# Kernel optimization log

Measured on AMD Instinct MI355X. Metric: run time of the kernel, lower is better.

Reference implementation:

```python
import jax, jax.numpy as jnp
import numpy as np

B, C, L, H = 8, 1024, 1024, 16
GROUPS = 32
EPS = 1e-5


def setup_inputs() -> dict:
    key = jax.random.key(0)
    ks = jax.random.split(key, 5)
    return {
        "x": jax.random.normal(ks[0], (B, C, L), dtype=jnp.float32),
        "norm_w": jnp.ones((C,), dtype=jnp.float32),
        "norm_b": jnp.zeros((C,), dtype=jnp.float32),
        "qkv_w": jax.random.normal(ks[1], (3 * C, C), dtype=jnp.float32) * (1.0 / np.sqrt(C)),
        "qkv_b": jax.random.normal(ks[2], (3 * C,), dtype=jnp.float32) * 0.02,
        "proj_w": jax.random.normal(ks[3], (C, C), dtype=jnp.float32) * (1.0 / np.sqrt(C)),
        "proj_b": jax.random.normal(ks[4], (C,), dtype=jnp.float32) * 0.02,
    }


def _group_norm(x, w, b):
    # x: [B, C, L]; GroupNorm over (channels-in-group, length)
    bs, c, l = x.shape
    xg = x.reshape(bs, GROUPS, c // GROUPS, l)
    mean = jnp.mean(xg, axis=(2, 3), keepdims=True)
    var = jnp.var(xg, axis=(2, 3), keepdims=True)
    xn = ((xg - mean) * jax.lax.rsqrt(var + EPS)).reshape(bs, c, l)
    return xn * w[None, :, None] + b[None, :, None]


def reference(x, norm_w, norm_b, qkv_w, qkv_b, proj_w, proj_b):
    b, c, l = x.shape
    ch = c // H  # per-head channels
    x_norm = _group_norm(x, norm_w, norm_b)
    # 1x1 conv == channel matmul: [B, 3C, L]
    qkv = jnp.einsum('oc,bcl->bol', qkv_w, x_norm) + qkv_b[None, :, None]
    # torch layout: reshape(bs*H, 3*ch, L) then split -> per-head [q; k; v]
    qkv = qkv.reshape(b * H, 3 * ch, l)
    q, k, v = qkv[:, :ch], qkv[:, ch:2 * ch], qkv[:, 2 * ch:]
    scale = 1.0 / np.sqrt(np.sqrt(ch))
    # explicit [b*H, L, L] score matrix, softmax in fp32 (matches .float())
    weight = jnp.einsum('bct,bcs->bts', q * scale, k * scale)
    weight = jax.nn.softmax(weight.astype(jnp.float32), axis=-1)
    a = jnp.einsum('bts,bcs->bct', weight, v.astype(jnp.float32))
    h = a.reshape(b, c, l).astype(x.dtype)
    h = jnp.einsum('oc,bcl->bol', proj_w, h) + proj_b[None, :, None]
    return x_norm + h  # tortoise_norm=False branch
```

## Files before the change

### kernel.cpp

```cpp
#include <hip/hip_runtime.h>
#include <cstdint>
#include <cstddef>

#define B_   8
#define C_   1024
#define L_   1024
#define H_   16
#define CH_  64
#define NG_  32
#define CPG_ 32

typedef __bf16 bf16;
typedef _Float16 f16;
typedef bf16  bf16x8 __attribute__((ext_vector_type(8)));
typedef bf16  bf16x4 __attribute__((ext_vector_type(4)));
typedef f16   f16x4  __attribute__((ext_vector_type(4)));
typedef f16   f16x2  __attribute__((ext_vector_type(2)));
typedef float f32x4  __attribute__((ext_vector_type(4)));

#define QSCALE 0.1803368801111203f

__device__ __forceinline__ void async_cp16(void* lds, const void* g) {
  __builtin_amdgcn_global_load_lds((__attribute__((address_space(1))) void*)g,
                                   (__attribute__((address_space(3))) void*)lds,
                                   16, 0, 0);
}

__device__ __forceinline__ f16x2 pk_f16(float a, float b) {
  return __builtin_bit_cast(f16x2, __builtin_amdgcn_cvt_pkrtz(a, b));
}

__device__ __forceinline__ int sw64(int r, int c) {
  return r * 64 + ((c ^ (r & 7)) << 3);
}

__global__ __launch_bounds__(256) void cvt_bf16_kernel(const float* __restrict__ src,
                                                       bf16* __restrict__ dst, int n4) {
  int i = blockIdx.x * 256 + threadIdx.x;
  if (i < n4) {
    float4 f = reinterpret_cast<const float4*>(src)[i];
    bf16x4 o;
    o[0] = (bf16)f.x; o[1] = (bf16)f.y; o[2] = (bf16)f.z; o[3] = (bf16)f.w;
    reinterpret_cast<bf16x4*>(dst)[i] = o;
  }
}

__global__ __launch_bounds__(256) void gn_stats_kernel(const float* __restrict__ x,
                                                       float* __restrict__ stats) {
  const int bg = blockIdx.x >> 3, sl = blockIdx.x & 7;
  const int tid = threadIdx.x;
  const float* xs = x + (size_t)bg * CPG_ * L_;
  const int c = tid >> 3;
  const int lbase = sl * 128 + (tid & 7) * 4;

  float s = 0.f, s2 = 0.f;
  #pragma unroll
  for (int t = 0; t < 4; t++) {
    float4 f = *reinterpret_cast<const float4*>(xs + (size_t)c * L_ + lbase + t * 32);
    s  += f.x + f.y + f.z + f.w;
    s2 += f.x * f.x + f.y * f.y + f.z * f.z + f.w * f.w;
  }
  __shared__ float rs[256], rs2[256];
  rs[tid] = s; rs2[tid] = s2;
  __syncthreads();
  for (int d = 128; d > 0; d >>= 1) {
    if (tid < d) { rs[tid] += rs[tid + d]; rs2[tid] += rs2[tid + d]; }
    __syncthreads();
  }
  if (tid == 0) {
    atomicAdd(&stats[bg * 2],     rs[0]);
    atomicAdd(&stats[bg * 2 + 1], rs2[0]);
  }
}

__global__ __launch_bounds__(256) void gn_apply_kernel(const float* __restrict__ x,
                                                       const float* __restrict__ gw,
                                                       const float* __restrict__ gb,
                                                       const float* __restrict__ stats,
                                                       bf16* __restrict__ xnb,
                                                       bf16* __restrict__ xT) {
  const int bg = blockIdx.x >> 2, l0 = (blockIdx.x & 3) * 256;
  const int b = bg >> 5, g = bg & 31;
  const int tid = threadIdx.x;
  const float* xs = x + (size_t)bg * CPG_ * L_;

  const float mean = stats[bg * 2] * (1.f / 32768.f);
  const float var  = stats[bg * 2 + 1] * (1.f / 32768.f) - mean * mean;
  const float inv  = rsqrtf(var + 1e-5f);

  __shared__ float tile[CPG_][257];
  #pragma unroll 4
  for (int c = 0; c < CPG_; c++) {
    const int gc = g * CPG_ + c;
    const float y = (xs[(size_t)c * L_ + l0 + tid] - mean) * inv * gw[gc] + gb[gc];
    xnb[(size_t)(b * C_ + gc) * L_ + l0 + tid] = (bf16)y;
    tile[c][tid] = y;
  }
  __syncthreads();
  const int c2 = tid & 31, lw = tid >> 5;
  #pragma unroll 4
  for (int jj = 0; jj < 32; jj++) {
    const int l = l0 + jj * 8 + lw;
    xT[(size_t)(b * L_ + l) * C_ + g * CPG_ + c2] = (bf16)tile[c2][jj * 8 + lw];
  }
}

__device__ __forceinline__ void gemm128_bt(const bf16* __restrict__ A,
                                           const bf16* __restrict__ Bt,
                                           int lda, int ldb, int K,
                                           int m0, int n0,
                                           bf16* As, bf16* Bs,
                                           f32x4 acc[4][4]) {
  const int tid  = threadIdx.x;
  const int wave = tid >> 6, lane = tid & 63;
  const int wm = (wave >> 1) * 64, wn = (wave & 1) * 64;
  const int l4 = lane & 15, quad = lane >> 4;
  const int rsub = lane >> 3;
  const int csrc = (((lane & 7) ^ rsub) << 3);

  const bf16* ga = A  + (size_t)(m0 + rsub) * lda + csrc;
  const bf16* gb = Bt + (size_t)(n0 + rsub) * ldb + csrc;

  for (int k0 = 0; k0 < K; k0 += 64) {
    __syncthreads();
    #pragma unroll
    for (int i = wave; i < 16; i += 4) {
      async_cp16(As + i * 512, ga + (size_t)(i * 8) * lda + k0);
      async_cp16(Bs + i * 512, gb + (size_t)(i * 8) * ldb + k0);
    }
    __syncthreads();

    #pragma unroll
    for (int kk = 0; kk < 2; kk++) {
      bf16x8 af[4], bfv[4];
      #pragma unroll
      for (int i = 0; i < 4; i++) {
        af[i] = *reinterpret_cast<const bf16x8*>(As + sw64(wm + i * 16 + l4, kk * 4 + quad));
      }
      #pragma unroll
      for (int j = 0; j < 4; j++) {
        bfv[j] = *reinterpret_cast<const bf16x8*>(Bs + sw64(wn + j * 16 + l4, kk * 4 + quad));
      }
      #pragma unroll
      for (int i = 0; i < 4; i++) {
        #pragma unroll
        for (int j = 0; j < 4; j++) {
          acc[i][j] = __builtin_amdgcn_mfma_f32_16x16x32_bf16(af[i], bfv[j], acc[i][j], 0, 0, 0);
        }
      }
    }
  }
}

__global__ __launch_bounds__(256) void qkv_gemm_kernel(const bf16* __restrict__ Wq,
                                                       const bf16* __restrict__ xT,
                                                       const float* __restrict__ bias,
                                                       bf16* __restrict__ qT,
                                                       bf16* __restrict__ kT,
                                                       f16* __restrict__ vB) {
  __shared__ bf16 As[128 * 64], Bs[128 * 64];
  const int bi = blockIdx.z;
  const int m0 = blockIdx.y * 128, n0 = blockIdx.x * 128;

  f32x4 acc[4][4];
  #pragma unroll
  for (int i = 0; i < 4; i++) {
    #pragma unroll
    for (int j = 0; j < 4; j++) { acc[i][j] = (f32x4){0.f, 0.f, 0.f, 0.f}; }
  }

  gemm128_bt(Wq, xT + (size_t)bi * L_ * C_, C_, C_, C_, m0, n0, As, Bs, acc);

  const int tid = threadIdx.x;
  const int wave = tid >> 6, lane = tid & 63;
  const int wm = (wave >> 1) * 64, wn = (wave & 1) * 64;
  const int l4 = lane & 15, quad = lane >> 4;

  #pragma unroll
  for (int i = 0; i < 4; i++) {
    const int ob = m0 + wm + i * 16 + quad * 4;
    const int h = ob / 192, r = ob % 192;
    const int sec = r >> 6, c = r & 63;
    float bb[4];
    #pragma unroll
    for (int rg = 0; rg < 4; rg++) { bb[rg] = bias[ob + rg]; }
    #pragma unroll
    for (int j = 0; j < 4; j++) {
      const int l = n0 + wn + j * 16 + l4;
      f32x4 a = acc[i][j];
      if (sec == 2) {
        const int e = l & 63, g64 = l >> 6;
        #pragma unroll
        for (int rg = 0; rg < 4; rg++) {
          const int cc = c + rg;
          const int ep = ((((e >> 2) ^ cc) & 15) << 2) | (e & 3);
          vB[(size_t)((bi * H_ + h) * CH_ + cc) * L_ + (g64 << 6) + ep] =
              (f16)(a[rg] + bb[rg]);
        }
      } else {
        const float sc = (sec == 0) ? QSCALE : 1.0f;
        bf16* dst = (sec == 0 ? qT : kT) + (size_t)((bi * H_ + h) * L_ + l) * CH_ + c;
        bf16x4 o;
        #pragma unroll
        for (int rg = 0; rg < 4; rg++) { o[rg] = (bf16)((a[rg] + bb[rg]) * sc); }
        *reinterpret_cast<bf16x4*>(dst) = o;
      }
    }
  }
}

__global__ __launch_bounds__(256, 4) void attn_kernel(const bf16* __restrict__ qT,
                                                      const bf16* __restrict__ kT,
                                                      const f16* __restrict__ vB,
                                                      bf16* __restrict__ aT) {
  const int tid = threadIdx.x, wave = tid >> 6, lane = tid & 63;
  const int l4 = lane & 15, quad = lane >> 4;
  const int rsub = lane >> 3;
  const int csrc = ((lane & 7) ^ rsub) << 3;

  __shared__ char smem[32768];

  const int tile = blockIdx.x;
  const int t0 = (tile & 7) * 128;
  const int hb = tile >> 3;
  const bf16* q = qT + (size_t)hb * L_ * CH_;
  const bf16* k = kT + (size_t)hb * L_ * CH_;
  const f16*  v = vB + (size_t)hb * CH_ * L_;

  {
    const bf16* gq = q + (size_t)t0 * CH_;
    #pragma unroll
    for (int i = wave; i < 16; i += 4) {
      async_cp16(smem + 16384 + i * 1024, gq + (i * 8 + rsub) * 64 + csrc);
    }
    #pragma unroll
    for (int i = wave; i < 8; i += 4) {
      async_cp16(smem + i * 1024, k + (size_t)(i * 8 + rsub) * 64 + csrc);
      async_cp16(smem + 8192 + i * 1024, v + (size_t)(i * 8 + rsub) * L_ + ((lane & 7) << 3));
    }
  }
  __syncthreads();

  bf16x8 bq0[2], bq1[2];
  {
    const bf16* qs = (const bf16*)(smem + 16384);
    #pragma unroll
    for (int u = 0; u < 2; u++) {
      bq0[u] = *reinterpret_cast<const bf16x8*>(qs + sw64(wave * 32 + u * 16 + l4, quad));
      bq1[u] = *reinterpret_cast<const bf16x8*>(qs + sw64(wave * 32 + u * 16 + l4, quad + 4));
    }
  }
  __syncthreads();

  f32x4 oacc[2][4];
  f32x4 lacc[2];
  float m_s[2];
  #pragma unroll
  for (int u = 0; u < 2; u++) {
    #pragma unroll
    for (int ct = 0; ct < 4; ct++) { oacc[u][ct] = (f32x4){0.f, 0.f, 0.f, 0.f}; }
    lacc[u] = (f32x4){0.f, 0.f, 0.f, 0.f};
    m_s[u] = -1e30f;
  }

  const f16x4 vone = {(f16)1.f, (f16)1.f, (f16)1.f, (f16)1.f};

  for (int it = 0; it < 16; it++) {
    const int cur = it & 1;
    if (it < 15) {
      const int s1 = (it + 1) * 64;
      char* nb = smem + (cur ^ 1) * 16384;
      const bf16* gk = k + (size_t)s1 * CH_;
      const f16*  gv = v + s1;
      #pragma unroll
      for (int i = wave; i < 8; i += 4) {
        async_cp16(nb + i * 1024, gk + (size_t)(i * 8 + rsub) * 64 + csrc);
        async_cp16(nb + 8192 + i * 1024, gv + (size_t)(i * 8 + rsub) * L_ + ((lane & 7) << 3));
      }
    }
    const bf16* ksc = (const bf16*)(smem + cur * 16384);
    const f16*  vsc = (const f16*)(smem + cur * 16384 + 8192);

    f32x4 st[2][4];
    #pragma unroll
    for (int j = 0; j < 4; j++) {
      const bf16x8 ak0 = *reinterpret_cast<const bf16x8*>(ksc + sw64(j * 16 + l4, quad));
      const bf16x8 ak1 = *reinterpret_cast<const bf16x8*>(ksc + sw64(j * 16 + l4, quad + 4));
      #pragma unroll
      for (int u = 0; u < 2; u++) {
        f32x4 z = (f32x4){0.f, 0.f, 0.f, 0.f};
        z = __builtin_amdgcn_mfma_f32_16x16x32_bf16(ak0, bq0[u], z, 0, 0, 0);
        z = __builtin_amdgcn_mfma_f32_16x16x32_bf16(ak1, bq1[u], z, 0, 0, 0);
        st[u][j] = z;
      }
    }

    float alpha[2], mn[2];
    #pragma unroll
    for (int u = 0; u < 2; u++) {
      float mx = fmaxf(fmaxf(st[u][0][0], st[u][0][1]), fmaxf(st[u][0][2], st[u][0][3]));
      #pragma unroll
      for (int j = 1; j < 4; j++) {
        mx = fmaxf(mx, fmaxf(fmaxf(st[u][j][0], st[u][j][1]), fmaxf(st[u][j][2], st[u][j][3])));
      }
      mx = fmaxf(mx, __shfl_xor(mx, 16));
      mx = fmaxf(mx, __shfl_xor(mx, 32));
      mn[u] = fmaxf(m_s[u], mx);
      alpha[u] = __builtin_amdgcn_exp2f(m_s[u] - mn[u]);
      m_s[u] = mn[u];
    }

    if (__any(alpha[0] != 1.0f || alpha[1] != 1.0f)) {
      #pragma unroll
      for (int u = 0; u < 2; u++) {
        float ar[4];
        #pragma unroll
        for (int r = 0; r < 4; r++) { ar[r] = __shfl(alpha[u], quad * 4 + r); }
        #pragma unroll
        for (int ct = 0; ct < 4; ct++) {
          #pragma unroll
          for (int r = 0; r < 4; r++) { oacc[u][ct][r] *= ar[r]; }
        }
        #pragma unroll
        for (int r = 0; r < 4; r++) { lacc[u][r] *= ar[r]; }
      }
    }

    f16x4 pa[2][4];
    #pragma unroll
    for (int u = 0; u < 2; u++) {
      #pragma unroll
      for (int j = 0; j < 4; j++) {
        const float p0 = __builtin_amdgcn_exp2f(st[u][j][0] - mn[u]);
        const float p1 = __builtin_amdgcn_exp2f(st[u][j][1] - mn[u]);
        const float p2 = __builtin_amdgcn_exp2f(st[u][j][2] - mn[u]);
        const float p3 = __builtin_amdgcn_exp2f(st[u][j][3] - mn[u]);
        pa[u][j] = __builtin_shufflevector(pk_f16(p0, p1), pk_f16(p2, p3), 0, 1, 2, 3);
        lacc[u] = __builtin_amdgcn_mfma_f32_16x16x16f16(pa[u][j], vone, lacc[u], 0, 0, 0);
      }
    }

    #pragma unroll
    for (int ct = 0; ct < 4; ct++) {
      const int c = ct * 16 + l4;
      #pragma unroll
      for (int j = 0; j < 4; j++) {
        const f16x4 vb = *reinterpret_cast<const f16x4*>(
            vsc + c * 64 + (((4 * j + quad) ^ l4) << 2));
        #pragma unroll
        for (int u = 0; u < 2; u++) {
          oacc[u][ct] = __builtin_amdgcn_mfma_f32_16x16x16f16(pa[u][j], vb, oacc[u][ct], 0, 0, 0);
        }
      }
    }
    __syncthreads();
  }

  const int bi = hb >> 4, h = hb & 15;
  #pragma unroll
  for (int u = 0; u < 2; u++) {
    float linv[4];
    #pragma unroll
    for (int r = 0; r < 4; r++) { linv[r] = 1.f / lacc[u][r]; }
    #pragma unroll
    for (int ct = 0; ct < 4; ct++) {
      #pragma unroll
      for (int r = 0; r < 4; r++) {
        const int t = t0 + wave * 32 + u * 16 + quad * 4 + r;
        const int c = h * CH_ + ct * 16 + l4;
        aT[(size_t)(bi * L_ + t) * C_ + c] = (bf16)(oacc[u][ct][r] * linv[r]);
      }
    }
  }
}

__global__ __launch_bounds__(256) void proj_gemm_kernel(const bf16* __restrict__ Wp,
                                                        const bf16* __restrict__ aT,
                                                        const float* __restrict__ bias,
                                                        const bf16* __restrict__ xnb,
                                                        float* __restrict__ out) {
  __shared__ bf16 As[128 * 64], Bs[128 * 64];
  const int bi = blockIdx.z;
  const int m0 = blockIdx.y * 128, n0 = blockIdx.x * 128;

  f32x4 acc[4][4];
  #pragma unroll
  for (int i = 0; i < 4; i++) {
    #pragma unroll
    for (int j = 0; j < 4; j++) { acc[i][j] = (f32x4){0.f, 0.f, 0.f, 0.f}; }
  }

  gemm128_bt(Wp, aT + (size_t)bi * L_ * C_, C_, C_, C_, m0, n0, As, Bs, acc);

  const int tid = threadIdx.x;
  const int wave = tid >> 6, lane = tid & 63;
  const int wm = (wave >> 1) * 64, wn = (wave & 1) * 64;
  const int l4 = lane & 15, quad = lane >> 4;

  #pragma unroll
  for (int i = 0; i < 4; i++) {
    const int ob = m0 + wm + i * 16 + quad * 4;
    float bb[4];
    #pragma unroll
    for (int rg = 0; rg < 4; rg++) { bb[rg] = bias[ob + rg]; }
    #pragma unroll
    for (int j = 0; j < 4; j++) {
      const int l = n0 + wn + j * 16 + l4;
      #pragma unroll
      for (int rg = 0; rg < 4; rg++) {
        const size_t idx = (size_t)(bi * C_ + ob + rg) * L_ + l;
        out[idx] = acc[i][j][rg] + bb[rg] + (float)xnb[idx];
      }
    }
  }
}

extern "C" void kernel_launch(void* const* d_in, const int* in_sizes, int n_in,
                              void* d_out, int out_size, void* d_ws, size_t ws_size,
                              hipStream_t stream) {
  (void)in_sizes; (void)n_in; (void)out_size; (void)ws_size;
  const float* x      = (const float*)d_in[0];
  const float* norm_w = (const float*)d_in[1];
  const float* norm_b = (const float*)d_in[2];
  const float* qkv_w  = (const float*)d_in[3];
  const float* qkv_b  = (const float*)d_in[4];
  const float* proj_w = (const float*)d_in[5];
  const float* proj_b = (const float*)d_in[6];
  float* out = (float*)d_out;

  char* w = (char*)d_ws;
  auto alloc = [&](size_t bytes) {
    char* p = w;
    w += (bytes + 255) & ~(size_t)255;
    return p;
  };
  bf16*  xnb   = (bf16*)alloc((size_t)B_ * C_ * L_ * 2);
  bf16*  xT    = (bf16*)alloc((size_t)B_ * L_ * C_ * 2);
  bf16*  wq    = (bf16*)alloc((size_t)3 * C_ * C_ * 2);
  bf16*  wp    = (bf16*)alloc((size_t)C_ * C_ * 2);
  bf16*  qT    = (bf16*)alloc((size_t)B_ * H_ * L_ * CH_ * 2);
  bf16*  kT    = (bf16*)alloc((size_t)B_ * H_ * L_ * CH_ * 2);
  f16*   vB    = (f16*)alloc((size_t)B_ * H_ * CH_ * L_ * 2);
  bf16*  aTb   = (bf16*)alloc((size_t)B_ * L_ * C_ * 2);
  float* stats = (float*)alloc((size_t)B_ * NG_ * 2 * 4);

  (void)hipMemsetAsync(stats, 0, (size_t)B_ * NG_ * 2 * 4, stream);
  cvt_bf16_kernel<<<(3 * C_ * C_ / 4) / 256, 256, 0, stream>>>(qkv_w, wq, 3 * C_ * C_ / 4);
  cvt_bf16_kernel<<<(C_ * C_ / 4) / 256, 256, 0, stream>>>(proj_w, wp, C_ * C_ / 4);
  gn_stats_kernel<<<B_ * NG_ * 8, 256, 0, stream>>>(x, stats);
  gn_apply_kernel<<<B_ * NG_ * 4, 256, 0, stream>>>(x, norm_w, norm_b, stats, xnb, xT);
  qkv_gemm_kernel<<<dim3(L_ / 128, 3 * C_ / 128, B_), 256, 0, stream>>>(wq, xT, qkv_b, qT, kT, vB);
  attn_kernel<<<1024, 256, 0, stream>>>(qT, kT, vB, aTb);
  proj_gemm_kernel<<<dim3(L_ / 128, C_ / 128, B_), 256, 0, stream>>>(wp, aTb, proj_b, xnb, out);
}
```

Before: 266.8 us.

## Double-buffer GEMM LDS tiles with K=32 stages and prefetch next tile

The shared bf16 GEMM mainloop changes from single-buffered 64-wide K tiles to double-buffered 32-wide K tiles. The async global-to-LDS copy of the next tile is issued before the MFMAs on the current tile, and a new swizzle suits the 32-column layout. The kernels also declare a minimum of 4 blocks per CU in their launch bounds. The goal is to hide global load latency behind compute and drop one barrier per iteration, at the cost of twice as many loop iterations and tighter register limits.

Measured after the change: 279.1 us. 4.6% more time.

```diff
diff --git a/kernel.cpp b/kernel.cpp
--- a/kernel.cpp
+++ b/kernel.cpp
@@ -30,6 +30,9 @@
   return __builtin_bit_cast(f16x2, __builtin_amdgcn_cvt_pkrtz(a, b));
 }
 
+__device__ __forceinline__ int sw32(int r, int c) {
+  return r * 32 + ((c ^ ((r >> 1) & 3)) << 3);
+}
 __device__ __forceinline__ int sw64(int r, int c) {
   return r * 64 + ((c ^ (r & 7)) << 3);
 }
@@ -115,50 +118,58 @@
   const int wave = tid >> 6, lane = tid & 63;
   const int wm = (wave >> 1) * 64, wn = (wave & 1) * 64;
   const int l4 = lane & 15, quad = lane >> 4;
-  const int rsub = lane >> 3;
-  const int csrc = (((lane & 7) ^ rsub) << 3);
-
-  const bf16* ga = A  + (size_t)(m0 + rsub) * lda + csrc;
-  const bf16* gb = Bt + (size_t)(n0 + rsub) * ldb + csrc;
-
-  for (int k0 = 0; k0 < K; k0 += 64) {
+  const int srow = lane >> 2;
+  const int scol = (((lane & 3) ^ ((srow >> 1) & 3)) << 3);
+
+  const bf16* ga = A  + (size_t)(m0 + wave * 16 + srow) * lda + scol;
+  const bf16* gb = Bt + (size_t)(n0 + wave * 16 + srow) * ldb + scol;
+  const int woff = wave * 512;
+
+  async_cp16(As + woff,        ga);
+  async_cp16(As + 2048 + woff, ga + (size_t)64 * lda);
+  async_cp16(Bs + woff,        gb);
+  async_cp16(Bs + 2048 + woff, gb + (size_t)64 * ldb);
+  __syncthreads();
+
+  for (int k0 = 0; k0 < K; k0 += 32) {
+    const int cur = (k0 >> 5) & 1;
+    if (k0 + 32 < K) {
+      const int nxt = (cur ^ 1) * 4096;
+      async_cp16(As + nxt + woff,        ga + k0 + 32);
+      async_cp16(As + nxt + 2048 + woff, ga + (size_t)64 * lda + k0 + 32);
+      async_cp16(Bs + nxt + woff,        gb + k0 + 32);
+      async_cp16(Bs + nxt + 2048 + woff, gb + (size_t)64 * ldb + k0 + 32);
+    }
+    const bf16* Ac = As + cur * 4096;
+    const bf16* Bc = Bs + cur * 4096;
+
+    bf16x8 af[4], bfv[4];
+    #pragma unroll
+    for (int i = 0; i < 4; i++) {
+      af[i] = *reinterpret_cast<const bf16x8*>(Ac + sw32(wm + i * 16 + l4, quad));
+    }
+    #pragma unroll
+    for (int j = 0; j < 4; j++) {
+      bfv[j] = *reinterpret_cast<const bf16x8*>(Bc + sw32(wn + j * 16 + l4, quad));
+    }
+    #pragma unroll
+    for (int i = 0; i < 4; i++) {
+      #pragma unroll
+      for (int j = 0; j < 4; j++) {
+        acc[i][j] = __builtin_amdgcn_mfma_f32_16x16x32_bf16(af[i], bfv[j], acc[i][j], 0, 0, 0);
+      }
+    }
     __syncthreads();
-    #pragma unroll
-    for (int i = wave; i < 16; i += 4) {
-      async_cp16(As + i * 512, ga + (size_t)(i * 8) * lda + k0);
-      async_cp16(Bs + i * 512, gb + (size_t)(i * 8) * ldb + k0);
-    }
-    __syncthreads();
-
-    #pragma unroll
-    for (int kk = 0; kk < 2; kk++) {
-      bf16x8 af[4], bfv[4];
-      #pragma unroll
-      for (int i = 0; i < 4; i++) {
-        af[i] = *reinterpret_cast<const bf16x8*>(As + sw64(wm + i * 16 + l4, kk * 4 + quad));
-      }
-      #pragma unroll
-      for (int j = 0; j < 4; j++) {
-        bfv[j] = *reinterpret_cast<const bf16x8*>(Bs + sw64(wn + j * 16 + l4, kk * 4 + quad));
-      }
-      #pragma unroll
-      for (int i = 0; i < 4; i++) {
-        #pragma unroll
-        for (int j = 0; j < 4; j++) {
-          acc[i][j] = __builtin_amdgcn_mfma_f32_16x16x32_bf16(af[i], bfv[j], acc[i][j], 0, 0, 0);
-        }
-      }
-    }
-  }
-}
-
-__global__ __launch_bounds__(256) void qkv_gemm_kernel(const bf16* __restrict__ Wq,
-                                                       const bf16* __restrict__ xT,
-                                                       const float* __restrict__ bias,
-                                                       bf16* __restrict__ qT,
-                                                       bf16* __restrict__ kT,
-                                                       f16* __restrict__ vB) {
-  __shared__ bf16 As[128 * 64], Bs[128 * 64];
+  }
+}
+
+__global__ __launch_bounds__(256, 4) void qkv_gemm_kernel(const bf16* __restrict__ Wq,
+                                                          const bf16* __restrict__ xT,
+                                                          const float* __restrict__ bias,
+                                                          bf16* __restrict__ qT,
+                                                          bf16* __restrict__ kT,
+                                                          f16* __restrict__ vB) {
+  __shared__ bf16 As[2 * 128 * 32], Bs[2 * 128 * 32];
   const int bi = blockIdx.z;
   const int m0 = blockIdx.y * 128, n0 = blockIdx.x * 128;
 
@@ -374,12 +385,12 @@
   }
 }
 
-__global__ __launch_bounds__(256) void proj_gemm_kernel(const bf16* __restrict__ Wp,
-                                                        const bf16* __restrict__ aT,
-                                                        const float* __restrict__ bias,
-                                                        const bf16* __restrict__ xnb,
-                                                        float* __restrict__ out) {
-  __shared__ bf16 As[128 * 64], Bs[128 * 64];
+__global__ __launch_bounds__(256, 4) void proj_gemm_kernel(const bf16* __restrict__ Wp,
+                                                           const bf16* __restrict__ aT,
+                                                           const float* __restrict__ bias,
+                                                           const bf16* __restrict__ xnb,
+                                                           float* __restrict__ out) {
+  __shared__ bf16 As[2 * 128 * 32], Bs[2 * 128 * 32];
   const int bi = blockIdx.z;
   const int m0 = blockIdx.y * 128, n0 = blockIdx.x * 128;
 
```
